# Optimization experiments

Hardware: AMD Instinct MI355X
Metric: run time of the kernel (lower is better)

## Reference

```python
import jax, jax.numpy as jnp
import numpy as np

PAD = 0
C_CONST = 0.1712209


def setup_inputs() -> dict:
    key = jax.random.key(0)
    ks = jax.random.split(key, 6)
    tlen, bsz, slen, hsize, vocab = 64, 32, 64, 1024, 32000
    hidden = jax.random.normal(ks[0], (tlen, bsz, hsize), dtype=jnp.float32)
    context = jax.random.normal(ks[1], (slen, bsz, hsize), dtype=jnp.float32)
    src = jax.random.randint(ks[2], (bsz, slen), 0, vocab, dtype=jnp.int64)
    stdv = 1.0 / np.sqrt(hsize)
    W_gen = jax.random.uniform(ks[3], (vocab, hsize), dtype=jnp.float32, minval=-stdv, maxval=stdv)
    b_gen = jnp.zeros((vocab,), dtype=jnp.float32)
    # Xavier-like init for the copy gate
    w_copy = jax.random.normal(ks[4], (hsize,), dtype=jnp.float32) * np.sqrt(2.0 / (hsize + 1))
    b_copy = jnp.zeros((1,), dtype=jnp.float32)
    return {"hidden": hidden, "context": context, "src": src,
            "W_gen": W_gen, "b_gen": b_gen, "w_copy": w_copy, "b_copy": b_copy}


def reference(hidden, context, src, W_gen, b_gen, w_copy, b_copy):
    tlen, bsz, hsize = hidden.shape
    # p(z=1): probability of copying, [tlen, bsz, 1]
    copy_prob = jax.nn.sigmoid(jnp.einsum('tbh,h->tb', hidden, w_copy) + b_copy[0])[..., None]
    # generator distribution over tgt vocab
    logits = jnp.einsum('tbh,vh->tbv', hidden, W_gen) + b_gen
    prob = jax.nn.softmax(logits.astype(jnp.float32), axis=-1)
    p_g = prob * (1.0 - copy_prob)  # [tlen, bsz, vocab]
    # copy attention over source positions: bmm(query[b,t,h], keys[b,s,h]^T)
    attn_score = jnp.einsum('tbh,sbh->bts', hidden, context)  # [bsz, tlen, slen]
    src_mask = (src == PAD)[:, None, :]  # [bsz, 1, slen]
    attn_score = jnp.where(src_mask, -jnp.inf, attn_score.astype(jnp.float32))
    attns = jax.nn.softmax(attn_score, axis=-1)  # [bsz, tlen, slen]
    p_c = jnp.transpose(attns, (1, 0, 2)) * copy_prob  # [tlen, bsz, slen]
    # scatter_add copy probs into vocab distribution along dim 2
    slen = src.shape[1]
    idx_src = jnp.broadcast_to(src[None, :, :], (tlen, bsz, slen))
    t_idx = jnp.arange(tlen)[:, None, None]
    b_idx = jnp.arange(bsz)[None, :, None]
    p_g = p_g.at[t_idx, b_idx, idx_src].add(p_c)
    return jnp.log(p_g) + C_CONST
```

## Files before the change

### kernel.cpp

```cpp
#include <hip/hip_runtime.h>
#include <hip/hip_bf16.h>
#include <stdint.h>

#define TLEN 64
#define BSZ 32
#define SLEN 64
#define HS 1024
#define VOC 32000
#define NROW (TLEN*BSZ)
#define C_CONST_F 0.1712209f

#define BM 256
#define BN 256
#define BKT 32
#define NKT (HS/BKT)
#define SLOT_BYTES 32768
#define B_REGION 16384

typedef __attribute__((ext_vector_type(8))) short short8;
typedef __attribute__((ext_vector_type(4))) float f32x4;

static __device__ __forceinline__ ushort f2bf(float f) {
    uint32_t u = __builtin_bit_cast(uint32_t, f);
    uint32_t r = (u + 0x7fffu + ((u >> 16) & 1u)) >> 16;
    return (ushort)r;
}
static __device__ __forceinline__ float bf2f(ushort u) {
    uint32_t v = ((uint32_t)u) << 16;
    return __builtin_bit_cast(float, v);
}
static __device__ __forceinline__ void async16(const void* g, void* lds) {
    __builtin_amdgcn_global_load_lds(
        (const __attribute__((address_space(1))) void*)g,
        (__attribute__((address_space(3))) void*)lds, 16, 0, 0);
}
static __device__ __forceinline__ int swz12(int e) { return e ^ (((e >> 4) & 15) << 1); }

__global__ __launch_bounds__(256) void gate_kernel(const float* __restrict__ hidden,
                                                   const float* __restrict__ w_copy,
                                                   const float* __restrict__ b_copy,
                                                   float* __restrict__ cp) {
    int wid = threadIdx.x >> 6, lane = threadIdx.x & 63;
    int row = blockIdx.x * 4 + wid;
    const float* h = hidden + (size_t)row * HS;
    float acc = 0.f;
    for (int i = 0; i < 4; ++i) {
        int off = (i * 64 + lane) * 4;
        float4 a = *(const float4*)(h + off);
        float4 w = *(const float4*)(w_copy + off);
        acc += a.x * w.x + a.y * w.y + a.z * w.z + a.w * w.w;
    }
    for (int m = 32; m >= 1; m >>= 1) acc += __shfl_xor(acc, m, 64);
    if (lane == 0) cp[row] = 1.f / (1.f + expf(-(acc + b_copy[0])));
}

__global__ __launch_bounds__(256) void attn_kernel(const float* __restrict__ hidden,
                                                   const float* __restrict__ context,
                                                   const int* __restrict__ src,
                                                   const float* __restrict__ cp,
                                                   float* __restrict__ p_c) {
    int row = blockIdx.x;
    int b = row & (BSZ - 1);
    int tid = threadIdx.x, wid = tid >> 6, lane = tid & 63;
    __shared__ float hrow[HS];
    __shared__ float sc[SLEN];
    *(float4*)(hrow + tid * 4) = *(const float4*)(hidden + (size_t)row * HS + tid * 4);
    __syncthreads();
    for (int j = 0; j < 16; ++j) {
        int s = wid * 16 + j;
        const float* c = context + ((size_t)s * BSZ + b) * HS;
        float acc = 0.f;
        for (int i = 0; i < 4; ++i) {
            int off = (i * 64 + lane) * 4;
            float4 cv = *(const float4*)(c + off);
            float4 hv = *(const float4*)(hrow + off);
            acc += cv.x * hv.x + cv.y * hv.y + cv.z * hv.z + cv.w * hv.w;
        }
        for (int m = 32; m >= 1; m >>= 1) acc += __shfl_xor(acc, m, 64);
        if (lane == 0) sc[s] = acc;
    }
    __syncthreads();
    if (tid < SLEN) {
        float v = sc[tid];
        if (src[b * SLEN + tid] == 0) v = -INFINITY;
        float m = v;
        for (int k = 32; k >= 1; k >>= 1) m = fmaxf(m, __shfl_xor(m, k, 64));
        float e = expf(v - m);
        float ssum = e;
        for (int k = 32; k >= 1; k >>= 1) ssum += __shfl_xor(ssum, k, 64);
        p_c[row * SLEN + tid] = (e / ssum) * cp[row];
    }
}

__global__ __launch_bounds__(256) void cvt_kernel(const float* __restrict__ in,
                                                  ushort* __restrict__ out, int n4) {
    int i = blockIdx.x * blockDim.x + threadIdx.x;
    if (i >= n4) return;
    float4 v = ((const float4*)in)[i];
    ushort4 o;
    o.x = f2bf(v.x); o.y = f2bf(v.y); o.z = f2bf(v.z); o.w = f2bf(v.w);
    ((ushort4*)out)[i] = o;
}

template <bool BF16L>
__global__ __launch_bounds__(512, 2) void gemm_kernel(const ushort* __restrict__ A,
                                                      const ushort* __restrict__ B,
                                                      const float* __restrict__ b_gen,
                                                      void* __restrict__ logits,
                                                      float* __restrict__ partials ) {
    __shared__ ushort sAB[4 * SLOT_BYTES / 2];

    int orig = blockIdx.x;
    int wg = (orig & 7) * 125 + (orig >> 3);
    int mIdx = wg & 7;
    int nIdx = wg >> 3;
    int m0 = mIdx * BM, n0 = nIdx * BN;
    int tid = threadIdx.x, wid = tid >> 6, lane = tid & 63;
    int wm = (wid >> 2) * 128, wn = (wid & 3) * 64;
    int lr = lane & 15, lg = lane >> 4;

    const ushort* gA[2]; const ushort* gB[2];
    uint32_t ldsOffA[2], ldsOffB[2];
    #pragma unroll
    for (int j = 0; j < 2; ++j) {
        int s = j * 512 + tid;
        int row = s >> 2;
        int kc = (s & 3) ^ ((row >> 1) & 3);
        gA[j] = A + (size_t)(m0 + row) * HS + kc * 8;
        gB[j] = B + (size_t)(n0 + row) * HS + kc * 8;
        ldsOffA[j] = (uint32_t)((j * 512 + wid * 64) * 16);
        ldsOffB[j] = (uint32_t)(B_REGION + (j * 512 + wid * 64) * 16);
    }

    uint32_t kcs   = (uint32_t)((lg ^ ((lr >> 1) & 3)) * 16);
    uint32_t offAb = (uint32_t)(wm + lr) * 64 + kcs;
    uint32_t offBb = B_REGION + (uint32_t)(wn + lr) * 64 + kcs;

    f32x4 acc[8][4];
    #pragma unroll
    for (int m = 0; m < 8; ++m)
        #pragma unroll
        for (int n = 0; n < 4; ++n) acc[m][n] = f32x4{0.f, 0.f, 0.f, 0.f};

    for (int kt = 0; kt < 3; ++kt) {
        char* sd = (char*)sAB + kt * SLOT_BYTES;
        int k0 = kt * BKT;
        #pragma unroll
        for (int j = 0; j < 2; ++j) {
            async16(gA[j] + k0, sd + ldsOffA[j]);
            async16(gB[j] + k0, sd + ldsOffB[j]);
        }
    }
    asm volatile("s_waitcnt vmcnt(8)" ::: "memory");
    asm volatile("s_barrier" ::: "memory");

#define KTILE(KT, DOSTAGE, VMASM)                                                      \
    {                                                                                  \
        const char* sl = (const char*)sAB + ((KT) & 3) * SLOT_BYTES;                   \
        short8 av[4], bv[4];                                                           \
        _Pragma("unroll")                                                              \
        for (int nb = 0; nb < 4; ++nb)                                                 \
            bv[nb] = *(const short8*)(sl + offBb + nb * 1024);                         \
        _Pragma("unroll")                                                              \
        for (int mb = 0; mb < 4; ++mb)                                                 \
            av[mb] = *(const short8*)(sl + offAb + mb * 1024);                         \
        if (DOSTAGE) {                                                                 \
            char* sd = (char*)sAB + (((KT) + 3) & 3) * SLOT_BYTES;                     \
            int k0s = ((KT) + 3) * BKT;                                                \
            async16(gA[0] + k0s, sd + ldsOffA[0]);                                     \
            async16(gB[0] + k0s, sd + ldsOffB[0]);                                     \
        }                                                                              \
        asm volatile("s_barrier" ::: "memory");                                        \
        asm volatile("s_waitcnt lgkmcnt(0)" ::: "memory");                             \
        __builtin_amdgcn_sched_barrier(0);                                             \
        __builtin_amdgcn_s_setprio(1);                                                 \
        _Pragma("unroll")                                                              \
        for (int mb = 0; mb < 4; ++mb)                                                 \
            _Pragma("unroll")                                                          \
            for (int nb = 0; nb < 4; ++nb)                                             \
                acc[mb][nb] = __builtin_amdgcn_mfma_f32_16x16x32_bf16(av[mb], bv[nb],  \
                                                                     acc[mb][nb], 0, 0, 0); \
        __builtin_amdgcn_s_setprio(0);                                                 \
        asm volatile("s_barrier" ::: "memory");                                        \
        _Pragma("unroll")                                                              \
        for (int mb = 0; mb < 4; ++mb)                                                 \
            av[mb] = *(const short8*)(sl + offAb + 4096 + mb * 1024);                  \
        if (DOSTAGE) {                                                                 \
            char* sd = (char*)sAB + (((KT) + 3) & 3) * SLOT_BYTES;                     \
            int k0s = ((KT) + 3) * BKT;                                                \
            async16(gA[1] + k0s, sd + ldsOffA[1]);                                     \
            async16(gB[1] + k0s, sd + ldsOffB[1]);                                     \
        }                                                                              \
        VMASM;                                                                         \
        asm volatile("s_barrier" ::: "memory");                                        \
        asm volatile("s_waitcnt lgkmcnt(0)" ::: "memory");                             \
        __builtin_amdgcn_sched_barrier(0);                                             \
        __builtin_amdgcn_s_setprio(1);                                                 \
        _Pragma("unroll")                                                              \
        for (int mb = 0; mb < 4; ++mb)                                                 \
            _Pragma("unroll")                                                          \
            for (int nb = 0; nb < 4; ++nb)                                             \
                acc[mb + 4][nb] = __builtin_amdgcn_mfma_f32_16x16x32_bf16(av[mb], bv[nb], \
                                                                     acc[mb + 4][nb], 0, 0, 0); \
        __builtin_amdgcn_s_setprio(0);                                                 \
        asm volatile("s_barrier" ::: "memory");                                        \
    }

    for (int kt = 0; kt < NKT - 3; ++kt) {
        KTILE(kt, true, asm volatile("s_waitcnt vmcnt(8)" ::: "memory"));
    }
    KTILE(NKT - 3, false, asm volatile("s_waitcnt vmcnt(4)" ::: "memory"));
    KTILE(NKT - 2, false, asm volatile("s_waitcnt vmcnt(0)" ::: "memory"));
    KTILE(NKT - 1, false, );
#undef KTILE

    float bg[4];
    #pragma unroll
    for (int nb = 0; nb < 4; ++nb) bg[nb] = b_gen[n0 + wn + nb * 16 + lr];
    int chunk = nIdx * 4 + (wid & 3);
    ushort* stile = sAB + wid * 8192;

    #pragma unroll
    for (int mb = 0; mb < 8; ++mb) {
        #pragma unroll
        for (int r = 0; r < 4; ++r) {
            int rl = mb * 16 + lg * 4 + r;
            int row = m0 + wm + rl;
            float v[4];
            float mx = -INFINITY;
            #pragma unroll
            for (int nb = 0; nb < 4; ++nb) {
                v[nb] = acc[mb][nb][r] + bg[nb];
                mx = fmaxf(mx, v[nb]);
            }
            if (BF16L) {
                #pragma unroll
                for (int nb = 0; nb < 4; ++nb) {
                    int cl = nb * 16 + lr;
                    int slot_w = (cl >> 3) ^ (rl & 7);
                    stile[rl * 64 + slot_w * 8 + (cl & 7)] = f2bf(v[nb]);
                }
            } else {
                float* outp = (float*)logits;
                #pragma unroll
                for (int nb = 0; nb < 4; ++nb)
                    outp[(size_t)row * VOC + n0 + wn + nb * 16 + lr] = v[nb];
            }
            for (int k = 8; k >= 1; k >>= 1) mx = fmaxf(mx, __shfl_xor(mx, k, 16));
            float se = 0.f;
            #pragma unroll
            for (int nb = 0; nb < 4; ++nb) se += __expf(v[nb] - mx);
            for (int k = 8; k >= 1; k >>= 1) se += __shfl_xor(se, k, 16);
            if (lr == 0) {
                float2 pv; pv.x = mx; pv.y = se;
                *(float2*)(partials + ((size_t)row * 500 + chunk) * 2) = pv;
            }
        }
    }
    if (BF16L) {
        ushort* Lbf = (ushort*)logits;
        #pragma unroll
        for (int rep = 0; rep < 16; ++rep) {
            int idx = rep * 64 + lane;
            int rl = idx >> 3, c8 = idx & 7;
            int slot_r = c8 ^ (rl & 7);
            short8 val = *(const short8*)(stile + rl * 64 + slot_r * 8);
            ushort* dst = Lbf + (size_t)(m0 + wm + rl) * VOC + n0 + wn + c8 * 8;
            *(short8*)dst = val;
        }
    }
}

__global__ __launch_bounds__(256) void reduce_kernel(const float* __restrict__ partials,
                                                     float* __restrict__ Ms,
                                                     float* __restrict__ Ss) {
    int wid = threadIdx.x >> 6, lane = threadIdx.x & 63;
    int row = blockIdx.x * 4 + wid;
    float m = -INFINITY, s = 0.f;
    for (int c = lane; c < 500; c += 64) {
        float2 p = *(const float2*)(partials + ((size_t)row * 500 + c) * 2);
        float nm = fmaxf(m, p.x);
        s = s * __expf(m - nm) + p.y * __expf(p.x - nm);
        m = nm;
    }
    for (int k = 32; k >= 1; k >>= 1) {
        float om = __shfl_xor(m, k, 64), os = __shfl_xor(s, k, 64);
        float nm = fmaxf(m, om);
        s = s * __expf(m - nm) + os * __expf(om - nm);
        m = nm;
    }
    if (lane == 0) { Ms[row] = m; Ss[row] = s; }
}

template <bool BF16L>
__global__ __launch_bounds__(256) void finalize_kernel(const int* __restrict__ src,
                                                       const float* __restrict__ p_c,
                                                       const float* __restrict__ cp,
                                                       const float* __restrict__ Ms,
                                                       const float* __restrict__ Ss,
                                                       const void* __restrict__ logits,
                                                       float* __restrict__ out) {
    int row = blockIdx.y;
    int c0 = blockIdx.x * 4096;
    int b = row & (BSZ - 1);
    __shared__ float addv[4096];
    int tid = threadIdx.x;
    for (int i = tid; i < 4096; i += 256) addv[i] = 0.f;
    __syncthreads();
    if (tid < SLEN) {
        int v = src[b * SLEN + tid];
        if (v >= c0 && v < c0 + 4096)
            atomicAdd(&addv[swz12(v - c0)], p_c[row * SLEN + tid]);
    }
    __syncthreads();
    int col = c0 + tid * 16;
    if (col >= VOC) return;
    float M = Ms[row];
    float g = (1.f - cp[row]) / Ss[row];
    float L[16];
    if (BF16L) {
        const ushort* lb = (const ushort*)logits + (size_t)row * VOC + col;
        short8 a = *(const short8*)lb;
        short8 c = *(const short8*)(lb + 8);
        for (int i = 0; i < 8; ++i) { L[i] = bf2f((ushort)a[i]); L[8 + i] = bf2f((ushort)c[i]); }
    } else {
        const float* lf = (const float*)logits + (size_t)row * VOC + col;
        for (int i = 0; i < 4; ++i) {
            float4 v = *(const float4*)(lf + i * 4);
            L[i * 4 + 0] = v.x; L[i * 4 + 1] = v.y; L[i * 4 + 2] = v.z; L[i * 4 + 3] = v.w;
        }
    }
    float res[16];
    for (int i = 0; i < 16; ++i) {
        float p = __expf(L[i] - M) * g + addv[swz12(tid * 16 + i)];
        res[i] = __logf(p) + C_CONST_F;
    }
    float* op = out + (size_t)row * VOC + col;
    for (int i = 0; i < 4; ++i) {
        float4 v;
        v.x = res[i * 4 + 0]; v.y = res[i * 4 + 1]; v.z = res[i * 4 + 2]; v.w = res[i * 4 + 3];
        *(float4*)(op + i * 4) = v;
    }
}

extern "C" void kernel_launch(void* const* d_in, const int* in_sizes, int n_in,
                              void* d_out, int out_size, void* d_ws, size_t ws_size,
                              hipStream_t stream) {
    const float* hidden  = (const float*)d_in[0];
    const float* context = (const float*)d_in[1];
    const int*   src     = (const int*)d_in[2];
    const float* W_gen   = (const float*)d_in[3];
    const float* b_gen   = (const float*)d_in[4];
    const float* w_copy  = (const float*)d_in[5];
    const float* b_copy  = (const float*)d_in[6];
    float* out = (float*)d_out;
    char* ws = (char*)d_ws;

    float*  cp       = (float*)(ws);
    float*  p_c      = (float*)(ws + 8192);
    float*  Ms       = (float*)(ws + 532480);
    float*  Ss       = (float*)(ws + 540672);
    float*  partials = (float*)(ws + 548864);
    ushort* Abf      = (ushort*)(ws + 8740864);
    ushort* Wbf      = (ushort*)(ws + 12935168);
    ushort* Lbf      = (ushort*)(ws + 78471168);
    const size_t NEED_BF16 = 209543168;

    gate_kernel<<<NROW / 4, 256, 0, stream>>>(hidden, w_copy, b_copy, cp);
    attn_kernel<<<NROW, 256, 0, stream>>>(hidden, context, src, cp, p_c);
    cvt_kernel<<<(NROW * HS / 4) / 256, 256, 0, stream>>>(hidden, Abf, NROW * HS / 4);
    cvt_kernel<<<(VOC * HS / 4) / 256, 256, 0, stream>>>(W_gen, Wbf, VOC * HS / 4);

    int ggrid = (NROW / BM) * (VOC / BN);
    dim3 fgrid(8, NROW);
    if (ws_size >= NEED_BF16) {
        gemm_kernel<true><<<ggrid, 512, 0, stream>>>(Abf, Wbf, b_gen, Lbf, partials);
        reduce_kernel<<<NROW / 4, 256, 0, stream>>>(partials, Ms, Ss);
        finalize_kernel<true><<<fgrid, 256, 0, stream>>>(src, p_c, cp, Ms, Ss, Lbf, out);
    } else {
        gemm_kernel<false><<<ggrid, 512, 0, stream>>>(Abf, Wbf, b_gen, out, partials);
        reduce_kernel<<<NROW / 4, 256, 0, stream>>>(partials, Ms, Ss);
        finalize_kernel<false><<<fgrid, 256, 0, stream>>>(src, p_c, cp, Ms, Ss, out, out);
    }
}
```

Before: 346.3 us.

## Shrink GEMM tile to 128x128 with 4 waves and simplified pipeline

Reduces the logits GEMM block tile from 256x256 with 8 waves to 128x128 with 4 waves. Each wave now holds a 64x64 accumulator. The two-half k-tile loop with mid-tile barriers becomes a single wait, barrier and MFMA phase per k-tile. This quadruples the grid and shrinks LDS per block, aiming for more resident blocks and better load balance. The cost is less operand reuse per loaded byte and more global and L2 traffic for A and W.

After: 385.6 us. 11.4% more time.

```diff
diff --git a/kernel.cpp b/kernel.cpp
--- a/kernel.cpp
+++ b/kernel.cpp
@@ -10,12 +10,12 @@
 #define NROW (TLEN*BSZ)
 #define C_CONST_F 0.1712209f
 
-#define BM 256
-#define BN 256
+#define BM 128
+#define BN 128
 #define BKT 32
 #define NKT (HS/BKT)
-#define SLOT_BYTES 32768
-#define B_REGION 16384
+#define SLOT_BYTES 16384
+#define B_REGION 8192
 
 typedef __attribute__((ext_vector_type(8))) short short8;
 typedef __attribute__((ext_vector_type(4))) float f32x4;
@@ -103,59 +103,62 @@
 }
 
 template <bool BF16L>
-__global__ __launch_bounds__(512, 2) void gemm_kernel(const ushort* __restrict__ A,
-                                                      const ushort* __restrict__ B,
-                                                      const float* __restrict__ b_gen,
-                                                      void* __restrict__ logits,
-                                                      float* __restrict__ partials ) {
+__global__ __launch_bounds__(256) void gemm_kernel(const ushort* __restrict__ A,
+                                                   const ushort* __restrict__ B,
+                                                   const float* __restrict__ b_gen,
+                                                   void* __restrict__ logits,
+                                                   float* __restrict__ partials ) {
     __shared__ ushort sAB[4 * SLOT_BYTES / 2];
 
     int orig = blockIdx.x;
-    int wg = (orig & 7) * 125 + (orig >> 3);
-    int mIdx = wg & 7;
-    int nIdx = wg >> 3;
+    int wg = (orig & 7) * 500 + (orig >> 3);
+    int mIdx = wg & 15;
+    int nIdx = wg >> 4;
     int m0 = mIdx * BM, n0 = nIdx * BN;
     int tid = threadIdx.x, wid = tid >> 6, lane = tid & 63;
-    int wm = (wid >> 2) * 128, wn = (wid & 3) * 64;
+    int wm = (wid >> 1) * 64, wn = (wid & 1) * 64;
     int lr = lane & 15, lg = lane >> 4;
 
     const ushort* gA[2]; const ushort* gB[2];
     uint32_t ldsOffA[2], ldsOffB[2];
     #pragma unroll
     for (int j = 0; j < 2; ++j) {
-        int s = j * 512 + tid;
+        int s = j * 256 + tid;
         int row = s >> 2;
         int kc = (s & 3) ^ ((row >> 1) & 3);
         gA[j] = A + (size_t)(m0 + row) * HS + kc * 8;
         gB[j] = B + (size_t)(n0 + row) * HS + kc * 8;
-        ldsOffA[j] = (uint32_t)((j * 512 + wid * 64) * 16);
-        ldsOffB[j] = (uint32_t)(B_REGION + (j * 512 + wid * 64) * 16);
+        ldsOffA[j] = (uint32_t)((j * 256 + wid * 64) * 16);
+        ldsOffB[j] = (uint32_t)(B_REGION + (j * 256 + wid * 64) * 16);
     }
 
     uint32_t kcs   = (uint32_t)((lg ^ ((lr >> 1) & 3)) * 16);
     uint32_t offAb = (uint32_t)(wm + lr) * 64 + kcs;
     uint32_t offBb = B_REGION + (uint32_t)(wn + lr) * 64 + kcs;
 
-    f32x4 acc[8][4];
+    f32x4 acc[4][4];
     #pragma unroll
-    for (int m = 0; m < 8; ++m)
+    for (int m = 0; m < 4; ++m)
         #pragma unroll
         for (int n = 0; n < 4; ++n) acc[m][n] = f32x4{0.f, 0.f, 0.f, 0.f};
 
-    for (int kt = 0; kt < 3; ++kt) {
-        char* sd = (char*)sAB + kt * SLOT_BYTES;
-        int k0 = kt * BKT;
-        #pragma unroll
-        for (int j = 0; j < 2; ++j) {
-            async16(gA[j] + k0, sd + ldsOffA[j]);
-            async16(gB[j] + k0, sd + ldsOffB[j]);
-        }
-    }
-    asm volatile("s_waitcnt vmcnt(8)" ::: "memory");
-    asm volatile("s_barrier" ::: "memory");
+#define STAGE(KT)                                                          \
+    {                                                                      \
+        char* sd = (char*)sAB + ((KT) & 3) * SLOT_BYTES;                   \
+        int k0s = (KT) * BKT;                                              \
+        _Pragma("unroll")                                                  \
+        for (int j = 0; j < 2; ++j) {                                      \
+            async16(gA[j] + k0s, sd + ldsOffA[j]);                         \
+            async16(gB[j] + k0s, sd + ldsOffB[j]);                         \
+        }                                                                  \
+    }
+
+    STAGE(0); STAGE(1); STAGE(2);
 
 #define KTILE(KT, DOSTAGE, VMASM)                                                      \
     {                                                                                  \
+        VMASM;                                                                         \
+        asm volatile("s_barrier" ::: "memory");                                        \
         const char* sl = (const char*)sAB + ((KT) & 3) * SLOT_BYTES;                   \
         short8 av[4], bv[4];                                                           \
         _Pragma("unroll")                                                              \
@@ -164,13 +167,7 @@
         _Pragma("unroll")                                                              \
         for (int mb = 0; mb < 4; ++mb)                                                 \
             av[mb] = *(const short8*)(sl + offAb + mb * 1024);                         \
-        if (DOSTAGE) {                                                                 \
-            char* sd = (char*)sAB + (((KT) + 3) & 3) * SLOT_BYTES;                     \
-            int k0s = ((KT) + 3) * BKT;                                                \
-            async16(gA[0] + k0s, sd + ldsOffA[0]);                                     \
-            async16(gB[0] + k0s, sd + ldsOffB[0]);                                     \
-        }                                                                              \
-        asm volatile("s_barrier" ::: "memory");                                        \
+        if (DOSTAGE) STAGE((KT) + 3);                                                  \
         asm volatile("s_waitcnt lgkmcnt(0)" ::: "memory");                             \
         __builtin_amdgcn_sched_barrier(0);                                             \
         __builtin_amdgcn_s_setprio(1);                                                 \
@@ -181,47 +178,27 @@
                 acc[mb][nb] = __builtin_amdgcn_mfma_f32_16x16x32_bf16(av[mb], bv[nb],  \
                                                                      acc[mb][nb], 0, 0, 0); \
         __builtin_amdgcn_s_setprio(0);                                                 \
-        asm volatile("s_barrier" ::: "memory");                                        \
-        _Pragma("unroll")                                                              \
-        for (int mb = 0; mb < 4; ++mb)                                                 \
-            av[mb] = *(const short8*)(sl + offAb + 4096 + mb * 1024);                  \
-        if (DOSTAGE) {                                                                 \
-            char* sd = (char*)sAB + (((KT) + 3) & 3) * SLOT_BYTES;                     \
-            int k0s = ((KT) + 3) * BKT;                                                \
-            async16(gA[1] + k0s, sd + ldsOffA[1]);                                     \
-            async16(gB[1] + k0s, sd + ldsOffB[1]);                                     \
-        }                                                                              \
-        VMASM;                                                                         \
-        asm volatile("s_barrier" ::: "memory");                                        \
-        asm volatile("s_waitcnt lgkmcnt(0)" ::: "memory");                             \
-        __builtin_amdgcn_sched_barrier(0);                                             \
-        __builtin_amdgcn_s_setprio(1);                                                 \
-        _Pragma("unroll")                                                              \
-        for (int mb = 0; mb < 4; ++mb)                                                 \
-            _Pragma("unroll")                                                          \
-            for (int nb = 0; nb < 4; ++nb)                                             \
-                acc[mb + 4][nb] = __builtin_amdgcn_mfma_f32_16x16x32_bf16(av[mb], bv[nb], \
-                                                                     acc[mb + 4][nb], 0, 0, 0); \
-        __builtin_amdgcn_s_setprio(0);                                                 \
-        asm volatile("s_barrier" ::: "memory");                                        \
     }
 
     for (int kt = 0; kt < NKT - 3; ++kt) {
         KTILE(kt, true, asm volatile("s_waitcnt vmcnt(8)" ::: "memory"));
     }
-    KTILE(NKT - 3, false, asm volatile("s_waitcnt vmcnt(4)" ::: "memory"));
-    KTILE(NKT - 2, false, asm volatile("s_waitcnt vmcnt(0)" ::: "memory"));
-    KTILE(NKT - 1, false, );
+    KTILE(NKT - 3, false, asm volatile("s_waitcnt vmcnt(8)" ::: "memory"));
+    KTILE(NKT - 2, false, asm volatile("s_waitcnt vmcnt(4)" ::: "memory"));
+    KTILE(NKT - 1, false, asm volatile("s_waitcnt vmcnt(0)" ::: "memory"));
 #undef KTILE
+#undef STAGE
+
+    asm volatile("s_barrier" ::: "memory");
 
     float bg[4];
     #pragma unroll
     for (int nb = 0; nb < 4; ++nb) bg[nb] = b_gen[n0 + wn + nb * 16 + lr];
-    int chunk = nIdx * 4 + (wid & 3);
-    ushort* stile = sAB + wid * 8192;
+    int chunk = nIdx * 2 + (wid & 1);
+    ushort* stile = sAB + wid * 4096;
 
     #pragma unroll
-    for (int mb = 0; mb < 8; ++mb) {
+    for (int mb = 0; mb < 4; ++mb) {
         #pragma unroll
         for (int r = 0; r < 4; ++r) {
             int rl = mb * 16 + lg * 4 + r;
@@ -260,7 +237,7 @@
     if (BF16L) {
         ushort* Lbf = (ushort*)logits;
         #pragma unroll
-        for (int rep = 0; rep < 16; ++rep) {
+        for (int rep = 0; rep < 8; ++rep) {
             int idx = rep * 64 + lane;
             int rl = idx >> 3, c8 = idx & 7;
             int slot_r = c8 ^ (rl & 7);
@@ -374,11 +351,11 @@
     int ggrid = (NROW / BM) * (VOC / BN);
     dim3 fgrid(8, NROW);
     if (ws_size >= NEED_BF16) {
-        gemm_kernel<true><<<ggrid, 512, 0, stream>>>(Abf, Wbf, b_gen, Lbf, partials);
+        gemm_kernel<true><<<ggrid, 256, 0, stream>>>(Abf, Wbf, b_gen, Lbf, partials);
         reduce_kernel<<<NROW / 4, 256, 0, stream>>>(partials, Ms, Ss);
         finalize_kernel<true><<<fgrid, 256, 0, stream>>>(src, p_c, cp, Ms, Ss, Lbf, out);
     } else {
-        gemm_kernel<false><<<ggrid, 512, 0, stream>>>(Abf, Wbf, b_gen, out, partials);
+        gemm_kernel<false><<<ggrid, 256, 0, stream>>>(Abf, Wbf, b_gen, out, partials);
         reduce_kernel<<<NROW / 4, 256, 0, stream>>>(partials, Ms, Ss);
         finalize_kernel<false><<<fgrid, 256, 0, stream>>>(src, p_c, cp, Ms, Ss, out, out);
     }
```
